# Performance work log

Hardware: AMD Instinct MI355X
Metric: run time of the kernel (lower is better)

The kernel has to match this reference:

```python
import jax, jax.numpy as jnp
import numpy as np
import math

B, N, DIM = 4, 4096, 1024
HEADS, DHEAD, NRF = 16, 64, 64
STAB = 1e-6  # numerical_stabilizer


def setup_inputs() -> dict:
    key = jax.random.key(0)
    k1, k2, k3, k4 = jax.random.split(key, 4)
    x = jax.random.normal(k1, (B, N, DIM), dtype=jnp.float32)
    W_qkv = jax.random.normal(k2, (DIM, 3 * HEADS * DHEAD), dtype=jnp.float32) * (1.0 / math.sqrt(DIM))
    RF = jax.random.normal(k3, (HEADS, DHEAD, NRF), dtype=jnp.float32) / math.sqrt(NRF)
    W_out = jax.random.normal(k4, (HEADS * DHEAD, DIM), dtype=jnp.float32) * (1.0 / math.sqrt(HEADS * DHEAD))
    b_out = jnp.zeros((DIM,), dtype=jnp.float32)
    return {"x": x, "W_qkv": W_qkv, "RF": RF, "W_out": W_out, "b_out": b_out}


def _phi(t, RF):
    # kernel transformation: project onto random features, then ReLU (default kernel)
    return jax.nn.relu(jnp.einsum('bhnd,hdr->bhnr', t, RF))


def reference(x, W_qkv, RF, W_out, b_out):
    b, n, _ = x.shape
    qkv = x @ W_qkv                                  # [b, n, 3*h*d]
    q, k, v = jnp.split(qkv, 3, axis=-1)
    def to_heads(t):
        return t.reshape(b, n, HEADS, DHEAD).transpose(0, 2, 1, 3)  # [b,h,n,d]
    q, k, v = to_heads(q), to_heads(k), to_heads(v)

    phi_q = _phi(q, RF)                              # [b,h,n,r]
    phi_k = _phi(k, RF)                              # [b,h,n,r]

    # linear-complexity FAVOR+ attention
    kv = jnp.einsum('bhnr,bhnd->bhrd', phi_k, v)     # [b,h,r,d]
    out = jnp.einsum('bhnr,bhrd->bhnd', phi_q, kv)   # [b,h,n,d]
    # normalizer: einsum('bhnr,bhmr->bhn') == phi_q @ sum_m(phi_k)
    k_sum = phi_k.sum(axis=2)                        # [b,h,r]
    normalizer = jnp.einsum('bhnr,bhr->bhn', phi_q, k_sum)[..., None] + STAB
    out = out / normalizer

    out = out.transpose(0, 2, 1, 3).reshape(b, n, HEADS * DHEAD)
    out = out @ W_out + b_out
    return out
```

## Files before the change

### kernel.cpp

```cpp
#include <hip/hip_runtime.h>


typedef __attribute__((ext_vector_type(8))) short s8v;
typedef __attribute__((ext_vector_type(4))) short s4v;
typedef __attribute__((ext_vector_type(4))) float f4v;
typedef __attribute__((ext_vector_type(4))) int   i4v;

#define MFMA16(a, b, c) __builtin_amdgcn_mfma_f32_16x16x32_bf16((a), (b), (c), 0, 0, 0)

__device__ __forceinline__ unsigned short f2bf(float f) {
  unsigned int u = __builtin_bit_cast(unsigned int, f);
  unsigned int r = (u + 0x7FFFu + ((u >> 16) & 1u)) >> 16;
  return (unsigned short)r;
}

__device__ __forceinline__ int swz(int p) {
  return p ^ (((p >> 7) & 7) << 4);
}

__device__ __forceinline__ void gl_lds16(const void* g, void* l) {
  __builtin_amdgcn_global_load_lds(
      (const __attribute__((address_space(1))) void*)g,
      (__attribute__((address_space(3))) void*)l, 16, 0, 0);
}

__global__ __launch_bounds__(256) void prep_all(const float* __restrict__ x,
                                                unsigned short* __restrict__ xb,
                                                const float* __restrict__ W_qkv,
                                                unsigned short* __restrict__ wqkvt,
                                                const float* __restrict__ W_out,
                                                unsigned short* __restrict__ woutt,
                                                const float* __restrict__ RF,
                                                unsigned short* __restrict__ rft) {
  const int b = blockIdx.x, t = threadIdx.x;
  __shared__ float tile[32][33];
  if (b < 16384) {
    int i = b * 256 + t;
    f4v v = ((const f4v*)x)[i];
    s4v o;
#pragma unroll
    for (int j = 0; j < 4; ++j) o[j] = (short)f2bf(v[j]);
    ((s4v*)xb)[i] = o;
    return;
  }
  const float* in;
  unsigned short* out;
  int R, C, bx, by;
  if (b < 19456) {
    int idx = b - 16384;
    in = W_qkv; out = wqkvt; R = 1024; C = 3072; bx = idx % 96; by = idx / 96;
  } else if (b < 20480) {
    int idx = b - 19456;
    in = W_out; out = woutt; R = 1024; C = 1024; bx = idx & 31; by = idx >> 5;
  } else {
    int idx = b - 20480;
    in = RF + (idx >> 2) * 4096; out = rft + (idx >> 2) * 4096;
    R = 64; C = 64; bx = idx & 1; by = (idx >> 1) & 1;
  }
  const int tx = t & 31, ty = t >> 5;
  const int c0 = bx * 32, r0 = by * 32;
#pragma unroll
  for (int j = 0; j < 4; ++j)
    tile[ty + j * 8][tx] = in[(size_t)(r0 + ty + j * 8) * C + c0 + tx];
  __syncthreads();
#pragma unroll
  for (int j = 0; j < 4; ++j)
    out[(size_t)(c0 + ty + j * 8) * R + r0 + tx] = f2bf(tile[tx][ty + j * 8]);
}

template <int MODE>
__global__ __launch_bounds__(512, 2) void gemm256(const unsigned short* __restrict__ A,
                                                  const unsigned short* __restrict__ Bt,
                                                  void* __restrict__ Cout,
                                                  const float* __restrict__ bias,
                                                  int Nn, int K, int NTN, int CPX) {
  __shared__ __align__(128) unsigned short smem[65536];
  const int t = threadIdx.x, w = t >> 6, lane = t & 63;
  const int wm = w >> 2, wn = w & 3;
  const int fr = lane & 15, c16 = (lane >> 4) * 16;
  const int nkt = K >> 6;

  const int bid = blockIdx.x;
  const int wg = (bid & 7) * CPX + (bid >> 3);
  const int tm = wg / NTN, tn = wg % NTN;

  const unsigned short* gA = A + (size_t)tm * 256 * K;
  const unsigned short* gB = Bt + (size_t)tn * 256 * K;

  const int s0 = swz(t * 16);
  const int s1 = swz(8192 + t * 16);
  const int goff0 = (s0 >> 7) * K + ((s0 & 127) >> 1);
  const int goff1 = ((s1 - 8192) >> 7) * K + ((s1 & 127) >> 1) + 64 * K;
  const int woff = w * 1024;

  auto stage = [&](int T2, int part) {
    if (T2 >= nkt) return;
    char* reg = (char*)smem + (((T2 & 1) * 4 + part) << 14);
    const unsigned short* gp =
        (part < 2 ? gA : gB) + (size_t)((part & 1) * 128) * K + T2 * 64;
    gl_lds16(gp + goff0, reg + woff);
    gl_lds16(gp + goff1, reg + 8192 + woff);
  };

  f4v acc[8][4] = {};
  stage(0, 0); stage(0, 1); stage(0, 2); stage(0, 3);

  auto rdA = [&](int mh, s8v (&a)[4][2], const char* Ar) {
#pragma unroll
    for (int i = 0; i < 4; ++i)
#pragma unroll
      for (int ks = 0; ks < 2; ++ks) {
        int p = swz((mh * 64 + i * 16 + fr) * 128 + ks * 64 + c16);
        a[i][ks] = *(const s8v*)(Ar + p);
      }
  };
  auto rdB = [&](int nh, s8v (&b)[2][2], const char* Br, int brow) {
#pragma unroll
    for (int j = 0; j < 2; ++j)
#pragma unroll
      for (int ks = 0; ks < 2; ++ks) {
        int p = swz((brow + nh * 32 + j * 16 + fr) * 128 + ks * 64 + c16);
        b[j][ks] = *(const s8v*)(Br + p);
      }
  };
  auto mmac = [&](int mh, int nh, const s8v (&a)[4][2], const s8v (&b)[2][2]) {
    __builtin_amdgcn_s_setprio(1);
#pragma unroll
    for (int i = 0; i < 4; ++i)
#pragma unroll
      for (int j = 0; j < 2; ++j) {
        acc[mh * 4 + i][nh * 2 + j] = MFMA16(a[i][0], b[j][0], acc[mh * 4 + i][nh * 2 + j]);
        acc[mh * 4 + i][nh * 2 + j] = MFMA16(a[i][1], b[j][1], acc[mh * 4 + i][nh * 2 + j]);
      }
    __builtin_amdgcn_s_setprio(0);
  };

  const int brow = (wn & 1) * 64;
  for (int T = 0; T < nkt; ++T) {
    const int d = T & 1;
    const char* Ar = (const char*)smem + ((d * 4 + wm) << 14);
    const char* Br = (const char*)smem + ((d * 4 + 2 + (wn >> 1)) << 14);
    asm volatile("s_waitcnt vmcnt(0)" ::: "memory");
    __builtin_amdgcn_s_barrier();
    __builtin_amdgcn_sched_barrier(0);
    stage(T + 1, 0); stage(T + 1, 1); stage(T + 1, 2); stage(T + 1, 3);
    s8v a[4][2], b0[2][2], b1[2][2];
    rdA(0, a, Ar); rdB(0, b0, Br, brow); rdB(1, b1, Br, brow);
    mmac(0, 0, a, b0);
    mmac(0, 1, a, b1);
    rdA(1, a, Ar);
    mmac(1, 1, a, b1);
    mmac(1, 0, a, b0);
  }

#pragma unroll
  for (int m = 0; m < 8; ++m)
#pragma unroll
    for (int n = 0; n < 4; ++n) {
      const int row = tm * 256 + wm * 128 + m * 16 + (lane >> 4) * 4;
      const int col = tn * 256 + wn * 64 + n * 16 + fr;
      if (MODE == 0) {
        unsigned short* C = (unsigned short*)Cout;
#pragma unroll
        for (int r = 0; r < 4; ++r)
          C[(size_t)(row + r) * Nn + col] = f2bf(acc[m][n][r]);
      } else {
        float* C = (float*)Cout;
        const float bv = bias[col];
#pragma unroll
        for (int r = 0; r < 4; ++r)
          C[(size_t)(row + r) * Nn + col] = acc[m][n][r] + bv;
      }
    }
}

__global__ __launch_bounds__(256) void phik_kv(const unsigned short* __restrict__ qkv,
                                               const unsigned short* __restrict__ RFt,
                                               float* __restrict__ kvpart) {
  __shared__ unsigned short RFl[2 * 64 * 32];
  __shared__ unsigned short Kl[2 * 128 * 32];
  __shared__ unsigned short pht[64 * 136];
  __shared__ unsigned short vt[80 * 136];
  const int t = threadIdx.x, w = t >> 6, lane = t & 63;
  const int och = blockIdx.x, h = blockIdx.y, b = blockIdx.z;
  const int fr = lane & 15, kg = (lane >> 4) * 8;

#pragma unroll
  for (int i = 0; i < 2; ++i) {
    int unit = i * 256 + w * 64 + lane;
    int p = unit >> 8, rem = unit & 255;
    int r = rem >> 2, cg = (rem & 3) * 8;
    gl_lds16(RFt + ((h * 64 + r) * 64 + p * 32 + cg), &RFl[(i * 256 + w * 64) * 8]);
  }
  for (int i = t; i < 136; i += 256) vt[64 * 136 + i] = 0x3F80;
  for (int i = t; i < 15 * 136; i += 256) vt[65 * 136 + i] = 0;

  f4v kvacc[5] = {};

  for (int c = 0; c < 4; ++c) {
    const int n0c = och * 512 + c * 128;
    const size_t rowbase = (size_t)(b * 4096 + n0c);
#pragma unroll
    for (int i = 0; i < 4; ++i) {
      int unit = i * 256 + w * 64 + lane;
      int p = unit >> 9, rem = unit & 511;
      int n = rem >> 2, cg = (rem & 3) * 8;
      gl_lds16(qkv + (rowbase + n) * 3072 + 1024 + h * 64 + p * 32 + cg,
               &Kl[(i * 256 + w * 64) * 8]);
    }
    i4v vreg[4];
#pragma unroll
    for (int it = 0; it < 4; ++it) {
      int slot = it * 256 + t;
      vreg[it] = *(const i4v*)&qkv[(rowbase + (slot >> 3)) * 3072 + 2048 + h * 64 +
                                   (slot & 7) * 8];
    }
    __syncthreads();
    f4v pacc[2][4] = {};
#pragma unroll
    for (int p = 0; p < 2; ++p) {
      s8v ka[2], rb[4];
#pragma unroll
      for (int m = 0; m < 2; ++m)
        ka[m] = *(const s8v*)&Kl[p * 4096 + (w * 32 + m * 16 + fr) * 32 + kg];
#pragma unroll
      for (int rf = 0; rf < 4; ++rf)
        rb[rf] = *(const s8v*)&RFl[p * 2048 + (rf * 16 + fr) * 32 + kg];
#pragma unroll
      for (int m = 0; m < 2; ++m)
#pragma unroll
        for (int rf = 0; rf < 4; ++rf)
          pacc[m][rf] = MFMA16(ka[m], rb[rf], pacc[m][rf]);
    }
#pragma unroll
    for (int it = 0; it < 4; ++it) {
      int slot = it * 256 + t;
      int vn = slot >> 3, key = slot & 7, vdh = key * 8;
      int cs = (((vn >> 3) ^ key) << 3) + (vn & 7);
      const unsigned short* vr = (const unsigned short*)&vreg[it];
#pragma unroll
      for (int j = 0; j < 8; ++j) vt[(vdh + j) * 136 + cs] = vr[j];
    }
#pragma unroll
    for (int m = 0; m < 2; ++m)
#pragma unroll
      for (int rf = 0; rf < 4; ++rf) {
        int r = rf * 16 + fr;
        int nb = w * 32 + m * 16 + (lane >> 4) * 4;
        int cs = (((nb >> 3) ^ ((r >> 3) & 7)) << 3) + (nb & 7);
        s4v pk;
#pragma unroll
        for (int g = 0; g < 4; ++g) pk[g] = (short)f2bf(fmaxf(pacc[m][rf][g], 0.0f));
        *(s4v*)&pht[r * 136 + cs] = pk;
      }
    __syncthreads();
#pragma unroll
    for (int kst = 0; kst < 4; ++kst) {
      const int ch = kst * 4 + (lane >> 4);
      const int prow = w * 16 + fr;
      s8v pb = *(const s8v*)&pht[prow * 136 + ((ch ^ ((prow >> 3) & 7)) << 3)];
#pragma unroll
      for (int f = 0; f < 5; ++f) {
        const int vrow = f * 16 + fr;
        s8v va = *(const s8v*)&vt[vrow * 136 + ((ch ^ ((vrow >> 3) & 7)) << 3)];
        kvacc[f] = MFMA16(va, pb, kvacc[f]);
      }
    }
  }
  const int bh = b * 16 + h;
  float* outp = kvpart + ((size_t)bh * 8 + och) * (80 * 64);
#pragma unroll
  for (int f = 0; f < 5; ++f) {
    int row = f * 16 + (lane >> 4) * 4;
    int col = w * 16 + fr;
#pragma unroll
    for (int g = 0; g < 4; ++g) outp[(row + g) * 64 + col] = kvacc[f][g];
  }
}

__global__ __launch_bounds__(256) void kv_reduce(const float* __restrict__ kvpart,
                                                 unsigned short* __restrict__ kvt) {
  const int bh = blockIdx.x, t = threadIdx.x;
  for (int i = t; i < 80 * 64; i += 256) {
    float s = 0.f;
#pragma unroll
    for (int c = 0; c < 8; ++c) s += kvpart[((size_t)bh * 8 + c) * 5120 + i];
    kvt[(size_t)bh * 5120 + i] = f2bf(s);
  }
}

__global__ __launch_bounds__(256) void phiq_out(const unsigned short* __restrict__ qkv,
                                                const unsigned short* __restrict__ RFt,
                                                const unsigned short* __restrict__ kvt,
                                                unsigned short* __restrict__ attno) {
  __shared__ unsigned short RFl[2 * 64 * 32];
  __shared__ unsigned short Ql[2 * 128 * 32];
  __shared__ unsigned short phl[128 * 72];
  __shared__ unsigned short kvl[80 * 72];
  const int t = threadIdx.x, w = t >> 6, lane = t & 63;
  const int ch = blockIdx.x, h = blockIdx.y, b = blockIdx.z;
  const int fr = lane & 15, kg = (lane >> 4) * 8;
  const int bh = b * 16 + h;
  const size_t rowbase = (size_t)(b * 4096 + ch * 128);

#pragma unroll
  for (int i = 0; i < 2; ++i) {
    int unit = i * 256 + w * 64 + lane;
    int p = unit >> 8, rem = unit & 255;
    int r = rem >> 2, cg = (rem & 3) * 8;
    gl_lds16(RFt + ((h * 64 + r) * 64 + p * 32 + cg), &RFl[(i * 256 + w * 64) * 8]);
  }
#pragma unroll
  for (int i = 0; i < 4; ++i) {
    int unit = i * 256 + w * 64 + lane;
    int p = unit >> 9, rem = unit & 511;
    int n = rem >> 2, cg = (rem & 3) * 8;
    gl_lds16(qkv + (rowbase + n) * 3072 + h * 64 + p * 32 + cg,
             &Ql[(i * 256 + w * 64) * 8]);
  }
  for (int i = t; i < 640; i += 256) {
    int row = i >> 3, cg = (i & 7) * 8;
    *(i4v*)&kvl[row * 72 + cg] = *(const i4v*)&kvt[(size_t)bh * 5120 + row * 64 + cg];
  }
  __syncthreads();
  f4v pacc[2][4] = {};
#pragma unroll
  for (int p = 0; p < 2; ++p) {
    s8v qa[2], rb[4];
#pragma unroll
    for (int m = 0; m < 2; ++m)
      qa[m] = *(const s8v*)&Ql[p * 4096 + (w * 32 + m * 16 + fr) * 32 + kg];
#pragma unroll
    for (int rf = 0; rf < 4; ++rf)
      rb[rf] = *(const s8v*)&RFl[p * 2048 + (rf * 16 + fr) * 32 + kg];
#pragma unroll
    for (int m = 0; m < 2; ++m)
#pragma unroll
      for (int rf = 0; rf < 4; ++rf)
        pacc[m][rf] = MFMA16(qa[m], rb[rf], pacc[m][rf]);
  }
#pragma unroll
  for (int m = 0; m < 2; ++m)
#pragma unroll
    for (int rf = 0; rf < 4; ++rf) {
      int r = rf * 16 + fr;
      int nb = w * 32 + m * 16 + (lane >> 4) * 4;
#pragma unroll
      for (int g = 0; g < 4; ++g) {
        int row = nb + g;
        int cs = (((r >> 3) ^ ((row >> 3) & 7)) << 3) + (r & 7);
        phl[row * 72 + cs] = f2bf(fmaxf(pacc[m][rf][g], 0.0f));
      }
    }
  __syncthreads();
  f4v acc[2][5] = {};
#pragma unroll
  for (int kst = 0; kst < 2; ++kst) {
    const int chk = kst * 4 + (lane >> 4);
    s8v pa[2], kb[5];
#pragma unroll
    for (int m = 0; m < 2; ++m) {
      int row = w * 32 + m * 16 + fr;
      pa[m] = *(const s8v*)&phl[row * 72 + ((chk ^ ((row >> 3) & 7)) << 3)];
    }
#pragma unroll
    for (int f = 0; f < 5; ++f)
      kb[f] = *(const s8v*)&kvl[(f * 16 + fr) * 72 + kst * 32 + kg];
#pragma unroll
    for (int m = 0; m < 2; ++m)
#pragma unroll
      for (int f = 0; f < 5; ++f) acc[m][f] = MFMA16(pa[m], kb[f], acc[m][f]);
  }
#pragma unroll
  for (int m = 0; m < 2; ++m)
#pragma unroll
    for (int g = 0; g < 4; ++g) {
      float nrm = __shfl(acc[m][4][g], lane & 48) + 1e-6f;
      int n = w * 32 + m * 16 + (lane >> 4) * 4 + g;
      size_t orow = rowbase + n;
#pragma unroll
      for (int f = 0; f < 4; ++f)
        attno[orow * 1024 + h * 64 + f * 16 + fr] = f2bf(acc[m][f][g] / nrm);
    }
}

extern "C" void kernel_launch(void* const* d_in, const int* in_sizes, int n_in,
                              void* d_out, int out_size, void* d_ws, size_t ws_size,
                              hipStream_t stream) {
  const float* x = (const float*)d_in[0];
  const float* W_qkv = (const float*)d_in[1];
  const float* RF = (const float*)d_in[2];
  const float* W_out = (const float*)d_in[3];
  const float* b_out = (const float*)d_in[4];
  float* out = (float*)d_out;

  char* ws = (char*)d_ws;
  size_t off = 0;
  auto alloc = [&](size_t bytes) -> void* {
    void* p = ws + off;
    off += (bytes + 255) & ~(size_t)255;
    return p;
  };
  unsigned short* xb = (unsigned short*)alloc(16384ull * 1024 * 2);
  unsigned short* wqkvt = (unsigned short*)alloc(3072ull * 1024 * 2);
  unsigned short* woutt = (unsigned short*)alloc(1024ull * 1024 * 2);
  unsigned short* rft = (unsigned short*)alloc(16ull * 64 * 64 * 2);
  unsigned short* qkv = (unsigned short*)alloc(16384ull * 3072 * 2);
  float* kvpart = (float*)alloc(64ull * 8 * 80 * 64 * 4);
  unsigned short* kvt = (unsigned short*)alloc(64ull * 80 * 64 * 2);
  unsigned short* attno = (unsigned short*)alloc(16384ull * 1024 * 2);

  prep_all<<<20544, 256, 0, stream>>>(x, xb, W_qkv, wqkvt, W_out, woutt, RF, rft);

  gemm256<0><<<768, 512, 0, stream>>>(xb, wqkvt, qkv, nullptr, 3072, 1024, 12, 96);
  phik_kv<<<dim3(8, 16, 4), 256, 0, stream>>>(qkv, rft, kvpart);
  kv_reduce<<<64, 256, 0, stream>>>(kvpart, kvt);
  phiq_out<<<dim3(32, 16, 4), 256, 0, stream>>>(qkv, rft, kvt, attno);
  gemm256<1><<<256, 512, 0, stream>>>(attno, woutt, out, b_out, 1024, 1024, 4, 32);
}
```

Before: 209.7 us.

## Restructure GEMM to 4 waves with 128x128 per-wave tiles

The 256x256 GEMM block now runs 4 waves instead of 8. Each wave computes a 128x128 output sub-tile with a 8x8 grid of MFMA accumulators, so every LDS fragment read is reused across more MFMAs. Staging now issues 16 global-to-LDS loads per thread per k-step into a simpler contiguous A/B buffer layout. In exchange, each wave holds 256 accumulator floats plus larger fragment arrays, which raises register pressure and allows only one block per CU, leaving less latency hiding.

```diff
diff --git a/kernel.cpp b/kernel.cpp
--- a/kernel.cpp
+++ b/kernel.cpp
@@ -69,14 +69,14 @@
 }
 
 template <int MODE>
-__global__ __launch_bounds__(512, 2) void gemm256(const unsigned short* __restrict__ A,
+__global__ __launch_bounds__(256, 1) void gemm256(const unsigned short* __restrict__ A,
                                                   const unsigned short* __restrict__ Bt,
                                                   void* __restrict__ Cout,
                                                   const float* __restrict__ bias,
                                                   int Nn, int K, int NTN, int CPX) {
   __shared__ __align__(128) unsigned short smem[65536];
   const int t = threadIdx.x, w = t >> 6, lane = t & 63;
-  const int wm = w >> 2, wn = w & 3;
+  const int wm = w >> 1, wn = w & 1;
   const int fr = lane & 15, c16 = (lane >> 4) * 16;
   const int nkt = K >> 6;
 
@@ -87,78 +87,62 @@
   const unsigned short* gA = A + (size_t)tm * 256 * K;
   const unsigned short* gB = Bt + (size_t)tn * 256 * K;
 
-  const int s0 = swz(t * 16);
-  const int s1 = swz(8192 + t * 16);
-  const int goff0 = (s0 >> 7) * K + ((s0 & 127) >> 1);
-  const int goff1 = ((s1 - 8192) >> 7) * K + ((s1 & 127) >> 1) + 64 * K;
-  const int woff = w * 1024;
-
-  auto stage = [&](int T2, int part) {
+  int goffs[8];
+#pragma unroll
+  for (int i = 0; i < 8; ++i) {
+    int o = i * 4096 + t * 16;
+    int s = swz(o);
+    goffs[i] = (s >> 7) * K + ((s & 127) >> 1);
+  }
+
+  auto stage = [&](int T2) {
     if (T2 >= nkt) return;
-    char* reg = (char*)smem + (((T2 & 1) * 4 + part) << 14);
-    const unsigned short* gp =
-        (part < 2 ? gA : gB) + (size_t)((part & 1) * 128) * K + T2 * 64;
-    gl_lds16(gp + goff0, reg + woff);
-    gl_lds16(gp + goff1, reg + 8192 + woff);
+    char* bufA = (char*)smem + (T2 & 1) * 65536;
+    char* bufB = bufA + 32768;
+    const unsigned short* gpA = gA + T2 * 64;
+    const unsigned short* gpB = gB + T2 * 64;
+#pragma unroll
+    for (int i = 0; i < 8; ++i) {
+      gl_lds16(gpA + goffs[i], bufA + i * 4096 + w * 1024);
+      gl_lds16(gpB + goffs[i], bufB + i * 4096 + w * 1024);
+    }
   };
 
-  f4v acc[8][4] = {};
-  stage(0, 0); stage(0, 1); stage(0, 2); stage(0, 3);
-
-  auto rdA = [&](int mh, s8v (&a)[4][2], const char* Ar) {
-#pragma unroll
-    for (int i = 0; i < 4; ++i)
-#pragma unroll
-      for (int ks = 0; ks < 2; ++ks) {
-        int p = swz((mh * 64 + i * 16 + fr) * 128 + ks * 64 + c16);
-        a[i][ks] = *(const s8v*)(Ar + p);
-      }
-  };
-  auto rdB = [&](int nh, s8v (&b)[2][2], const char* Br, int brow) {
-#pragma unroll
-    for (int j = 0; j < 2; ++j)
-#pragma unroll
-      for (int ks = 0; ks < 2; ++ks) {
-        int p = swz((brow + nh * 32 + j * 16 + fr) * 128 + ks * 64 + c16);
-        b[j][ks] = *(const s8v*)(Br + p);
-      }
-  };
-  auto mmac = [&](int mh, int nh, const s8v (&a)[4][2], const s8v (&b)[2][2]) {
-    __builtin_amdgcn_s_setprio(1);
-#pragma unroll
-    for (int i = 0; i < 4; ++i)
-#pragma unroll
-      for (int j = 0; j < 2; ++j) {
-        acc[mh * 4 + i][nh * 2 + j] = MFMA16(a[i][0], b[j][0], acc[mh * 4 + i][nh * 2 + j]);
-        acc[mh * 4 + i][nh * 2 + j] = MFMA16(a[i][1], b[j][1], acc[mh * 4 + i][nh * 2 + j]);
-      }
-    __builtin_amdgcn_s_setprio(0);
-  };
-
-  const int brow = (wn & 1) * 64;
+  f4v acc[8][8] = {};
+  stage(0);
+
   for (int T = 0; T < nkt; ++T) {
-    const int d = T & 1;
-    const char* Ar = (const char*)smem + ((d * 4 + wm) << 14);
-    const char* Br = (const char*)smem + ((d * 4 + 2 + (wn >> 1)) << 14);
+    const char* Ar = (const char*)smem + (T & 1) * 65536;
+    const char* Br = Ar + 32768;
     asm volatile("s_waitcnt vmcnt(0)" ::: "memory");
     __builtin_amdgcn_s_barrier();
     __builtin_amdgcn_sched_barrier(0);
-    stage(T + 1, 0); stage(T + 1, 1); stage(T + 1, 2); stage(T + 1, 3);
-    s8v a[4][2], b0[2][2], b1[2][2];
-    rdA(0, a, Ar); rdB(0, b0, Br, brow); rdB(1, b1, Br, brow);
-    mmac(0, 0, a, b0);
-    mmac(0, 1, a, b1);
-    rdA(1, a, Ar);
-    mmac(1, 1, a, b1);
-    mmac(1, 0, a, b0);
+    stage(T + 1);
+    s8v a[8][2], b[8][2];
+#pragma unroll
+    for (int i = 0; i < 8; ++i)
+#pragma unroll
+      for (int ks = 0; ks < 2; ++ks) {
+        a[i][ks] = *(const s8v*)(Ar + swz((wm * 128 + i * 16 + fr) * 128 + ks * 64 + c16));
+        b[i][ks] = *(const s8v*)(Br + swz((wn * 128 + i * 16 + fr) * 128 + ks * 64 + c16));
+      }
+    __builtin_amdgcn_s_setprio(1);
+#pragma unroll
+    for (int ks = 0; ks < 2; ++ks)
+#pragma unroll
+      for (int m = 0; m < 8; ++m)
+#pragma unroll
+        for (int n = 0; n < 8; ++n)
+          acc[m][n] = MFMA16(a[m][ks], b[n][ks], acc[m][n]);
+    __builtin_amdgcn_s_setprio(0);
   }
 
 #pragma unroll
   for (int m = 0; m < 8; ++m)
 #pragma unroll
-    for (int n = 0; n < 4; ++n) {
+    for (int n = 0; n < 8; ++n) {
       const int row = tm * 256 + wm * 128 + m * 16 + (lane >> 4) * 4;
-      const int col = tn * 256 + wn * 64 + n * 16 + fr;
+      const int col = tn * 256 + wn * 128 + n * 16 + fr;
       if (MODE == 0) {
         unsigned short* C = (unsigned short*)Cout;
 #pragma unroll
@@ -412,9 +396,9 @@
 
   prep_all<<<20544, 256, 0, stream>>>(x, xb, W_qkv, wqkvt, W_out, woutt, RF, rft);
 
-  gemm256<0><<<768, 512, 0, stream>>>(xb, wqkvt, qkv, nullptr, 3072, 1024, 12, 96);
+  gemm256<0><<<768, 256, 0, stream>>>(xb, wqkvt, qkv, nullptr, 3072, 1024, 12, 96);
   phik_kv<<<dim3(8, 16, 4), 256, 0, stream>>>(qkv, rft, kvpart);
   kv_reduce<<<64, 256, 0, stream>>>(kvpart, kvt);
   phiq_out<<<dim3(32, 16, 4), 256, 0, stream>>>(qkv, rft, kvt, attno);
-  gemm256<1><<<256, 512, 0, stream>>>(attno, woutt, out, b_out, 1024, 1024, 4, 32);
-}
+  gemm256<1><<<256, 256, 0, stream>>>(attno, woutt, out, b_out, 1024, 1024, 4, 32);
+}
```

Measured after the change: 217.9 us. 1.04x slower.

## Fuse fp32-to-bf16 conversion of x into QKV GEMM A-tile loading

Applied to the files above, without the earlier changes.

Removes the separate pass that converted x to bf16 in workspace; the QKV GEMM now loads fp32 A tiles into registers, converts them to bf16 and writes them to LDS while the B tile streams via direct global-to-LDS loads. This eliminates a full read/write/reread of the activation buffer. In exchange, the GEMM reads twice as many bytes for A per tile across column blocks, uses more registers for the staged A data, and adds an extra wait before each barrier.

```diff
diff --git a/kernel.cpp b/kernel.cpp
--- a/kernel.cpp
+++ b/kernel.cpp
@@ -24,9 +24,7 @@
       (__attribute__((address_space(3))) void*)l, 16, 0, 0);
 }
 
-__global__ __launch_bounds__(256) void prep_all(const float* __restrict__ x,
-                                                unsigned short* __restrict__ xb,
-                                                const float* __restrict__ W_qkv,
+__global__ __launch_bounds__(256) void prep_all(const float* __restrict__ W_qkv,
                                                 unsigned short* __restrict__ wqkvt,
                                                 const float* __restrict__ W_out,
                                                 unsigned short* __restrict__ woutt,
@@ -34,26 +32,16 @@
                                                 unsigned short* __restrict__ rft) {
   const int b = blockIdx.x, t = threadIdx.x;
   __shared__ float tile[32][33];
-  if (b < 16384) {
-    int i = b * 256 + t;
-    f4v v = ((const f4v*)x)[i];
-    s4v o;
-#pragma unroll
-    for (int j = 0; j < 4; ++j) o[j] = (short)f2bf(v[j]);
-    ((s4v*)xb)[i] = o;
-    return;
-  }
   const float* in;
   unsigned short* out;
   int R, C, bx, by;
-  if (b < 19456) {
-    int idx = b - 16384;
-    in = W_qkv; out = wqkvt; R = 1024; C = 3072; bx = idx % 96; by = idx / 96;
-  } else if (b < 20480) {
-    int idx = b - 19456;
+  if (b < 3072) {
+    in = W_qkv; out = wqkvt; R = 1024; C = 3072; bx = b % 96; by = b / 96;
+  } else if (b < 4096) {
+    int idx = b - 3072;
     in = W_out; out = woutt; R = 1024; C = 1024; bx = idx & 31; by = idx >> 5;
   } else {
-    int idx = b - 20480;
+    int idx = b - 4096;
     in = RF + (idx >> 2) * 4096; out = rft + (idx >> 2) * 4096;
     R = 64; C = 64; bx = idx & 1; by = (idx >> 1) & 1;
   }
@@ -70,6 +58,7 @@
 
 template <int MODE>
 __global__ __launch_bounds__(512, 2) void gemm256(const unsigned short* __restrict__ A,
+                                                  const float* __restrict__ Af,
                                                   const unsigned short* __restrict__ Bt,
                                                   void* __restrict__ Cout,
                                                   const float* __restrict__ bias,
@@ -85,25 +74,68 @@
   const int tm = wg / NTN, tn = wg % NTN;
 
   const unsigned short* gA = A + (size_t)tm * 256 * K;
+  const float* gAf = Af + (size_t)tm * 256 * K;
   const unsigned short* gB = Bt + (size_t)tn * 256 * K;
 
   const int s0 = swz(t * 16);
   const int s1 = swz(8192 + t * 16);
   const int goff0 = (s0 >> 7) * K + ((s0 & 127) >> 1);
-  const int goff1 = ((s1 - 8192) >> 7) * K + ((s1 & 127) >> 1) + 64 * K;
+  const int goff1 = (s1 >> 7) * K + ((s1 & 127) >> 1);
   const int woff = w * 1024;
 
-  auto stage = [&](int T2, int part) {
+  auto stageB = [&](int T2) {
     if (T2 >= nkt) return;
-    char* reg = (char*)smem + (((T2 & 1) * 4 + part) << 14);
-    const unsigned short* gp =
-        (part < 2 ? gA : gB) + (size_t)((part & 1) * 128) * K + T2 * 64;
-    gl_lds16(gp + goff0, reg + woff);
-    gl_lds16(gp + goff1, reg + 8192 + woff);
+#pragma unroll
+    for (int part = 2; part < 4; ++part) {
+      char* reg = (char*)smem + (((T2 & 1) * 4 + part) << 14);
+      const unsigned short* gp = gB + (size_t)((part & 1) * 128) * K + T2 * 64;
+      gl_lds16(gp + goff0, reg + woff);
+      gl_lds16(gp + goff1, reg + 8192 + woff);
+    }
+  };
+  auto stageA16 = [&](int T2) {
+    if (T2 >= nkt) return;
+#pragma unroll
+    for (int part = 0; part < 2; ++part) {
+      char* reg = (char*)smem + (((T2 & 1) * 4 + part) << 14);
+      const unsigned short* gp = gA + (size_t)((part & 1) * 128) * K + T2 * 64;
+      gl_lds16(gp + goff0, reg + woff);
+      gl_lds16(gp + goff1, reg + 8192 + woff);
+    }
+  };
+  f4v ar[8];
+  auto loadA = [&](int T2) {
+    if (T2 >= nkt) return;
+    const float* p0 = gAf + T2 * 64;
+#pragma unroll
+    for (int pt = 0; pt < 2; ++pt) {
+      const float* pp = p0 + (size_t)pt * 128 * K;
+      ar[pt * 4 + 0] = *(const f4v*)(pp + goff0);
+      ar[pt * 4 + 1] = *(const f4v*)(pp + goff0 + 4);
+      ar[pt * 4 + 2] = *(const f4v*)(pp + goff1);
+      ar[pt * 4 + 3] = *(const f4v*)(pp + goff1 + 4);
+    }
+  };
+  auto writeA = [&](int T2) {
+    if (T2 >= nkt) return;
+    char* base = (char*)smem + (((T2 & 1) * 4) << 14);
+#pragma unroll
+    for (int pt = 0; pt < 2; ++pt) {
+      char* pb = base + (pt << 14);
+      s8v o0, o1;
+#pragma unroll
+      for (int j = 0; j < 4; ++j) {
+        o0[j] = (short)f2bf(ar[pt * 4 + 0][j]);
+        o0[4 + j] = (short)f2bf(ar[pt * 4 + 1][j]);
+        o1[j] = (short)f2bf(ar[pt * 4 + 2][j]);
+        o1[4 + j] = (short)f2bf(ar[pt * 4 + 3][j]);
+      }
+      *(s8v*)(pb + t * 16) = o0;
+      *(s8v*)(pb + 8192 + t * 16) = o1;
+    }
   };
 
   f4v acc[8][4] = {};
-  stage(0, 0); stage(0, 1); stage(0, 2); stage(0, 3);
 
   auto rdA = [&](int mh, s8v (&a)[4][2], const char* Ar) {
 #pragma unroll
@@ -136,21 +168,52 @@
   };
 
   const int brow = (wn & 1) * 64;
-  for (int T = 0; T < nkt; ++T) {
-    const int d = T & 1;
-    const char* Ar = (const char*)smem + ((d * 4 + wm) << 14);
-    const char* Br = (const char*)smem + ((d * 4 + 2 + (wn >> 1)) << 14);
+
+  if constexpr (MODE == 0) {
+    loadA(0);
+    stageB(0);
     asm volatile("s_waitcnt vmcnt(0)" ::: "memory");
+    writeA(0);
+    asm volatile("s_waitcnt lgkmcnt(0)" ::: "memory");
     __builtin_amdgcn_s_barrier();
     __builtin_amdgcn_sched_barrier(0);
-    stage(T + 1, 0); stage(T + 1, 1); stage(T + 1, 2); stage(T + 1, 3);
-    s8v a[4][2], b0[2][2], b1[2][2];
-    rdA(0, a, Ar); rdB(0, b0, Br, brow); rdB(1, b1, Br, brow);
-    mmac(0, 0, a, b0);
-    mmac(0, 1, a, b1);
-    rdA(1, a, Ar);
-    mmac(1, 1, a, b1);
-    mmac(1, 0, a, b0);
+    for (int T = 0; T < nkt; ++T) {
+      const int d = T & 1;
+      const char* Ar = (const char*)smem + ((d * 4 + wm) << 14);
+      const char* Br = (const char*)smem + ((d * 4 + 2 + (wn >> 1)) << 14);
+      stageB(T + 1);
+      loadA(T + 1);
+      s8v a[4][2], b0[2][2], b1[2][2];
+      rdA(0, a, Ar); rdB(0, b0, Br, brow); rdB(1, b1, Br, brow);
+      mmac(0, 0, a, b0);
+      mmac(0, 1, a, b1);
+      rdA(1, a, Ar);
+      mmac(1, 1, a, b1);
+      mmac(1, 0, a, b0);
+      asm volatile("s_waitcnt vmcnt(0)" ::: "memory");
+      writeA(T + 1);
+      asm volatile("s_waitcnt lgkmcnt(0)" ::: "memory");
+      __builtin_amdgcn_s_barrier();
+      __builtin_amdgcn_sched_barrier(0);
+    }
+  } else {
+    stageA16(0); stageB(0);
+    for (int T = 0; T < nkt; ++T) {
+      const int d = T & 1;
+      const char* Ar = (const char*)smem + ((d * 4 + wm) << 14);
+      const char* Br = (const char*)smem + ((d * 4 + 2 + (wn >> 1)) << 14);
+      asm volatile("s_waitcnt vmcnt(0)" ::: "memory");
+      __builtin_amdgcn_s_barrier();
+      __builtin_amdgcn_sched_barrier(0);
+      stageA16(T + 1); stageB(T + 1);
+      s8v a[4][2], b0[2][2], b1[2][2];
+      rdA(0, a, Ar); rdB(0, b0, Br, brow); rdB(1, b1, Br, brow);
+      mmac(0, 0, a, b0);
+      mmac(0, 1, a, b1);
+      rdA(1, a, Ar);
+      mmac(1, 1, a, b1);
+      mmac(1, 0, a, b0);
+    }
   }
 
 #pragma unroll
@@ -401,7 +464,6 @@
     off += (bytes + 255) & ~(size_t)255;
     return p;
   };
-  unsigned short* xb = (unsigned short*)alloc(16384ull * 1024 * 2);
   unsigned short* wqkvt = (unsigned short*)alloc(3072ull * 1024 * 2);
   unsigned short* woutt = (unsigned short*)alloc(1024ull * 1024 * 2);
   unsigned short* rft = (unsigned short*)alloc(16ull * 64 * 64 * 2);
@@ -410,11 +472,13 @@
   unsigned short* kvt = (unsigned short*)alloc(64ull * 80 * 64 * 2);
   unsigned short* attno = (unsigned short*)alloc(16384ull * 1024 * 2);
 
-  prep_all<<<20544, 256, 0, stream>>>(x, xb, W_qkv, wqkvt, W_out, woutt, RF, rft);
-
-  gemm256<0><<<768, 512, 0, stream>>>(xb, wqkvt, qkv, nullptr, 3072, 1024, 12, 96);
+  prep_all<<<4160, 256, 0, stream>>>(W_qkv, wqkvt, W_out, woutt, RF, rft);
+
+  gemm256<0><<<768, 512, 0, stream>>>(nullptr, x, wqkvt, qkv, nullptr,
+                                      3072, 1024, 12, 96);
   phik_kv<<<dim3(8, 16, 4), 256, 0, stream>>>(qkv, rft, kvpart);
   kv_reduce<<<64, 256, 0, stream>>>(kvpart, kvt);
   phiq_out<<<dim3(32, 16, 4), 256, 0, stream>>>(qkv, rft, kvt, attno);
-  gemm256<1><<<256, 512, 0, stream>>>(attno, woutt, out, b_out, 1024, 1024, 4, 32);
-}
+  gemm256<1><<<256, 512, 0, stream>>>(attno, nullptr, woutt, out, b_out,
+                                      1024, 1024, 4, 32);
+}
```

Measured after the change: 269.0 us. +28.3%, slower.
